# Optimization experiments

Measured on AMD Instinct MI355X. Metric: run time of the kernel, lower is better.

Reference implementation:

```python
import jax, jax.numpy as jnp
import numpy as np
import math

B, L, D, P = 2, 2048, 256, 32
PI = math.pi


def _layernorm(x, g, b, eps=1e-5):
    m = x.mean(-1, keepdims=True)
    v = x.var(-1, keepdims=True)
    return (x - m) / jnp.sqrt(v + eps) * g + b


def setup_inputs() -> dict:
    key = jax.random.key(0)
    ks = jax.random.split(key, 16)
    sd = 1.0 / math.sqrt(D)
    f32 = jnp.float32
    inp = {
        "x": jax.random.normal(ks[0], (B, L, D), f32),
        # key_encoder: Linear(D, P)
        "key_W": jax.random.normal(ks[1], (D, P), f32) * sd,
        "key_b": jnp.zeros((P,), f32),
        # value_encoder: Linear(D, D)
        "val_W": jax.random.normal(ks[2], (D, D), f32) * sd,
        "val_b": jnp.zeros((D,), f32),
        # refiner: LayerNorm(D), Linear(D, 2D), GELU, Linear(2D, D)
        "ln1_g": jnp.ones((D,), f32),
        "ln1_b": jnp.zeros((D,), f32),
        "W1": jax.random.normal(ks[3], (D, 2 * D), f32) * sd,
        "b1": jnp.zeros((2 * D,), f32),
        "W2": jax.random.normal(ks[4], (2 * D, D), f32) * (1.0 / math.sqrt(2 * D)),
        "b2": jnp.zeros((D,), f32),
        # to_out: LayerNorm(D), Linear(D, D)
        "ln2_g": jnp.ones((D,), f32),
        "ln2_b": jnp.zeros((D,), f32),
        "Wo": jax.random.normal(ks[5], (D, D), f32) * sd,
        "bo": jnp.zeros((D,), f32),
    }
    return inp


def reference(x, key_W, key_b, val_W, val_b, ln1_g, ln1_b, W1, b1, W2, b2,
              ln2_g, ln2_b, Wo, bo):
    # key phases in (-pi, pi); phasor exp(i*theta) handled as (cos, sin)
    phases = jnp.tanh(x @ key_W + key_b) * PI          # (B, L, P)
    values = x @ val_W + val_b                          # (B, L, D)

    cos_p = jnp.cos(phases)
    sin_p = jnp.sin(phases)
    # torch.roll(shifts=1, dims=1) then zero the first position -> shift right, row 0 = 0
    zrow = jnp.zeros_like(cos_p[:, :1])
    cos_s = jnp.concatenate([zrow, cos_p[:, :-1]], axis=1)
    sin_s = jnp.concatenate([zrow, sin_p[:, :-1]], axis=1)

    # odd positions hold values
    vmask = (jnp.arange(L) % 2 == 1).astype(x.dtype)    # (L,)
    mv = values * vmask[None, :, None]                  # (B, L, D)

    # bind: outer product phasor (P) x value (D); real/imag parts
    bound_re = cos_s[..., None] * mv[:, :, None, :]     # (B, L, P, D)
    bound_im = sin_s[..., None] * mv[:, :, None, :]
    mem_re = jnp.cumsum(bound_re, axis=1)
    mem_im = jnp.cumsum(bound_im, axis=1)

    # retrieve: Re[ memory * exp(-i*theta) ] summed over phases
    retrieved = (jnp.einsum('blpd,blp->bld', mem_re, cos_p)
                 + jnp.einsum('blpd,blp->bld', mem_im, sin_p))

    valid = jnp.maximum(jnp.cumsum(vmask), 1.0)         # (L,)
    retrieved = retrieved / (jnp.sqrt(valid)[None, :, None] * math.sqrt(P))

    h = _layernorm(retrieved, ln1_g, ln1_b)
    h = jax.nn.gelu(h @ W1 + b1, approximate=False)
    refined = h @ W2 + b2
    out = x + (_layernorm(refined, ln2_g, ln2_b) @ Wo + bo)
    return out
```

## Files before the change

kernel.cpp:

```cpp
#include <hip/hip_runtime.h>
#include <math.h>

#define BB 2
#define LL 2048
#define DD 256
#define PP 32
#define NC 64
#define PI_F 3.14159265358979323846f

typedef __attribute__((ext_vector_type(8))) short bf16x8;
typedef __attribute__((ext_vector_type(4))) float f32x4;
typedef unsigned short ushort_t;
typedef unsigned int uint_t;

__device__ inline ushort_t f2bf(float x) {
    uint_t u = __float_as_uint(x);
    uint_t r = (u + 0x7fffu + ((u >> 16) & 1u)) >> 16;
    return (ushort_t)r;
}

__global__ __launch_bounds__(256) void prep_key_kernel(
    const float* __restrict__ W1, const float* __restrict__ W2,
    const float* __restrict__ Wo, const float* __restrict__ valW,
    const float* __restrict__ x, const float* __restrict__ key_W,
    const float* __restrict__ key_b,
    ushort_t* __restrict__ W1t, ushort_t* __restrict__ W2t,
    ushort_t* __restrict__ Wot, ushort_t* __restrict__ valWt,
    float2* __restrict__ ph)
{
    const int bid = blockIdx.x;
    const int t = threadIdx.x;
    if (bid < 96) {
        __shared__ float T[64][65];
        const float* W; ushort_t* Wt; int K, N, tile;
        if (bid < 32)      { W = W1;   Wt = W1t;   K = 256; N = 512; tile = bid; }
        else if (bid < 64) { W = W2;   Wt = W2t;   K = 512; N = 256; tile = bid - 32; }
        else if (bid < 80) { W = Wo;   Wt = Wot;   K = 256; N = 256; tile = bid - 64; }
        else               { W = valW; Wt = valWt; K = 256; N = 256; tile = bid - 80; }
        const int ntiles = N / 64;
        const int k0 = (tile / ntiles) * 64, n0 = (tile % ntiles) * 64;
        {
            const int rr = t >> 2, cb = (t & 3) * 16;
            #pragma unroll
            for (int i = 0; i < 16; i += 4) {
                const float4 v = *(const float4*)&W[(k0 + rr) * N + n0 + cb + i];
                T[rr][cb + i + 0] = v.x; T[rr][cb + i + 1] = v.y;
                T[rr][cb + i + 2] = v.z; T[rr][cb + i + 3] = v.w;
            }
        }
        __syncthreads();
        {
            const int n = t >> 2, kb = (t & 3) * 16;
            #pragma unroll
            for (int i = 0; i < 16; ++i)
                Wt[(n0 + n) * K + k0 + kb + i] = f2bf(T[kb + i][n]);
        }
    } else {
        __shared__ ushort_t xt[16][264];
        __shared__ ushort_t kwT[32][264];
        __shared__ float rbuf[4][2][16][17];
        const int row0 = (bid - 96) * 16;
        {
            const int l = t >> 4, cb = (t & 15) * 16;
            const float* src = &x[(long)(row0 + l) * DD + cb];
            ushort_t tmp[16];
            #pragma unroll
            for (int i = 0; i < 4; ++i) {
                const float4 v = *(const float4*)&src[i * 4];
                tmp[i*4+0] = f2bf(v.x); tmp[i*4+1] = f2bf(v.y);
                tmp[i*4+2] = f2bf(v.z); tmp[i*4+3] = f2bf(v.w);
            }
            *(uint4*)&xt[l][cb]     = *(uint4*)&tmp[0];
            *(uint4*)&xt[l][cb + 8] = *(uint4*)&tmp[8];
        }
        {
            #pragma unroll
            for (int i = 0; i < 8; ++i) {
                const int idx4 = i * 256 + t;
                const int k = idx4 >> 3, pc = (idx4 & 7) * 4;
                const float4 v = *(const float4*)&key_W[k * 32 + pc];
                kwT[pc + 0][k] = f2bf(v.x);
                kwT[pc + 1][k] = f2bf(v.y);
                kwT[pc + 2][k] = f2bf(v.z);
                kwT[pc + 3][k] = f2bf(v.w);
            }
        }
        __syncthreads();
        const int wv = t >> 6, lane = t & 63;
        const int qd = lane >> 4, mc = lane & 15;
        f32x4 acc0 = {0.f,0.f,0.f,0.f}, acc1 = {0.f,0.f,0.f,0.f};
        #pragma unroll
        for (int ks = 0; ks < 2; ++ks) {
            const int ko = wv * 64 + ks * 32 + qd * 8;
            const bf16x8 a  = *(const bf16x8*)&xt[mc][ko];
            const bf16x8 b0 = *(const bf16x8*)&kwT[mc][ko];
            const bf16x8 b1 = *(const bf16x8*)&kwT[16 + mc][ko];
            acc0 = __builtin_amdgcn_mfma_f32_16x16x32_bf16(a, b0, acc0, 0, 0, 0);
            acc1 = __builtin_amdgcn_mfma_f32_16x16x32_bf16(a, b1, acc1, 0, 0, 0);
        }
        #pragma unroll
        for (int r = 0; r < 4; ++r) {
            rbuf[wv][0][qd * 4 + r][mc] = acc0[r];
            rbuf[wv][1][qd * 4 + r][mc] = acc1[r];
        }
        __syncthreads();
        #pragma unroll
        for (int rep = 0; rep < 2; ++rep) {
            const int idx = rep * 256 + t;
            const int p = idx & 31, l = idx >> 5;
            const int nf = p >> 4, mcol = p & 15;
            float a = key_b[p] + rbuf[0][nf][l][mcol] + rbuf[1][nf][l][mcol]
                    + rbuf[2][nf][l][mcol] + rbuf[3][nf][l][mcol];
            a = tanhf(a) * PI_F;
            float sn, cs;
            sincosf(a, &sn, &cs);
            ph[(long)(row0 + l) * PP + p] = make_float2(cs, sn);
        }
    }
}

__global__ __launch_bounds__(256) void valbind_kernel(
    const float* __restrict__ x, const float2* __restrict__ ph,
    const ushort_t* __restrict__ valWt, const float* __restrict__ val_b,
    ushort_t* __restrict__ VoddT, float* __restrict__ Mt)
{
    __shared__ ushort_t xsb[16][264];
    __shared__ ushort_t VdT[64][40];
    __shared__ ushort_t phsT[64][40];
    __shared__ float    Ms[64][68];

    const int tid = threadIdx.x;
    const int bid = blockIdx.x;
    const int b  = bid >> 8;
    const int c  = (bid >> 2) & 63;
    const int dq = bid & 3;
    const int base = b * LL;
    const int r0 = 32 * c;

    {
        const int j = tid >> 4, cb = (tid & 15) * 16;
        const float* src = &x[(long)(base + r0 + 2 * j + 1) * DD + cb];
        ushort_t tmp[16];
        #pragma unroll
        for (int i = 0; i < 4; ++i) {
            const float4 v = *(const float4*)&src[i * 4];
            tmp[i*4+0] = f2bf(v.x); tmp[i*4+1] = f2bf(v.y);
            tmp[i*4+2] = f2bf(v.z); tmp[i*4+3] = f2bf(v.w);
        }
        *(uint4*)&xsb[j][cb]     = *(uint4*)&tmp[0];
        *(uint4*)&xsb[j][cb + 8] = *(uint4*)&tmp[8];
    }
    {
        const int j = tid >> 4, qb = (tid & 15) * 4;
        const float4 v = *(const float4*)((const float*)ph +
                              (long)(base + r0 + 2 * j) * 64 + qb);
        phsT[qb + 0][j] = f2bf(v.x);
        phsT[qb + 1][j] = f2bf(v.y);
        phsT[qb + 2][j] = f2bf(v.z);
        phsT[qb + 3][j] = f2bf(v.w);
    }
    for (int e = tid; e < 64 * 16; e += 256) {
        phsT[e >> 4][16 + (e & 15)] = 0;
        VdT[e >> 4][16 + (e & 15)] = 0;
    }
    __syncthreads();

    const int wv = tid >> 6, lane = tid & 63;
    const int qd = lane >> 4, mc = lane & 15;

    f32x4 va = {0.f,0.f,0.f,0.f};
    const int dloc = wv * 16 + mc;
    const int ng = dq * 64 + dloc;
    const ushort_t* B0 = &valWt[(long)ng * 256];
    #pragma unroll
    for (int ks = 0; ks < 8; ++ks) {
        const bf16x8 a  = *(const bf16x8*)&xsb[mc][ks * 32 + qd * 8];
        const bf16x8 b0 = *(const bf16x8*)&B0[ks * 32 + qd * 8];
        va = __builtin_amdgcn_mfma_f32_16x16x32_bf16(a, b0, va, 0, 0, 0);
    }
    {
        const float bb = val_b[ng];
        #pragma unroll
        for (int r = 0; r < 4; ++r)
            VdT[dloc][qd * 4 + r] = f2bf(va[r] + bb);
    }
    __syncthreads();

    const bf16x8 a2 = *(const bf16x8*)&phsT[wv * 16 + mc][qd * 8];
    f32x4 macc[4];
    #pragma unroll
    for (int nf = 0; nf < 4; ++nf) {
        f32x4 z = {0.f,0.f,0.f,0.f};
        const bf16x8 b2 = *(const bf16x8*)&VdT[nf * 16 + mc][qd * 8];
        macc[nf] = __builtin_amdgcn_mfma_f32_16x16x32_bf16(a2, b2, z, 0, 0, 0);
    }
    #pragma unroll
    for (int nf = 0; nf < 4; ++nf) {
        #pragma unroll
        for (int r = 0; r < 4; ++r)
            Ms[nf * 16 + mc][wv * 16 + qd * 4 + r] = macc[nf][r];
    }
    __syncthreads();

    {
        float* dst = &Mt[((long)(b * NC + c) * 256 + dq * 64) * 64];
        #pragma unroll
        for (int p = 0; p < 4; ++p) {
            const int idx4 = p * 256 + tid;
            const int dl = idx4 >> 4, q4 = (idx4 & 15) * 4;
            *(float4*)&dst[dl * 64 + q4] = *(const float4*)&Ms[dl][q4];
        }
    }
    if (tid < 64) {
        ushort_t* vd = &VoddT[((long)(b * NC + c) * 256 + dq * 64 + tid) * 16];
        *(uint4*)&vd[0] = *(const uint4*)&VdT[tid][0];
        *(uint4*)&vd[8] = *(const uint4*)&VdT[tid][8];
    }
}

__global__ __launch_bounds__(256) void prefix_kernel(
    const float* __restrict__ M, ushort_t* __restrict__ Mpre_b)
{
    __shared__ float segsum[4][64];
    const int tid = threadIdx.x;
    const int b  = blockIdx.x >> 8;
    const int cg = blockIdx.x & 255;
    const int col = cg * 64 + (tid & 63);
    const int seg = tid >> 6;
    const long base = (long)b * NC * 16384 + col;

    float v[16], s = 0.f;
    #pragma unroll
    for (int i = 0; i < 16; ++i) {
        v[i] = M[base + (long)(seg * 16 + i) * 16384];
        s += v[i];
    }
    segsum[seg][tid & 63] = s;
    __syncthreads();
    float run = 0.f;
    #pragma unroll
    for (int sg = 0; sg < 3; ++sg)
        if (sg < seg) run += segsum[sg][tid & 63];
    #pragma unroll
    for (int i = 0; i < 16; ++i) {
        const long a = base + (long)(seg * 16 + i) * 16384;
        Mpre_b[a] = f2bf(run);
        run += v[i];
    }
}

__global__ __launch_bounds__(256) void retrieve_mlp_kernel(
    const float* __restrict__ ph, const ushort_t* __restrict__ Mpre_b,
    const ushort_t* __restrict__ VoddT,
    const float* __restrict__ ln1_g, const float* __restrict__ ln1_b,
    const ushort_t* __restrict__ W1t, const float* __restrict__ b1,
    const ushort_t* __restrict__ W2t, const float* __restrict__ b2,
    const float* __restrict__ ln2_g, const float* __restrict__ ln2_b,
    const ushort_t* __restrict__ Wot, const float* __restrict__ bo,
    const float* __restrict__ x, float* __restrict__ out)
{
    __shared__ ushort_t Bs_m[256][72];
    __shared__ ushort_t Bs_v[256][32];
    __shared__ ushort_t As_ph[16][72];
    __shared__ ushort_t Bs_sh[16][72];
    __shared__ ushort_t As_p[16][32];
    __shared__ float    refct[16][264];
    __shared__ ushort_t rhat_s[16][264];
    __shared__ ushort_t h_s[16][520];
    __shared__ ushort_t shT[16][264];

    const int tid = threadIdx.x;
    const int b = blockIdx.x >> 7;
    const int c = (blockIdx.x >> 1) & 63;
    const int h = blockIdx.x & 1;
    const int l0g = 32 * c + 16 * h;
    const long rowbase = (long)b * LL + l0g;

    {
        const ushort_t* src = &Mpre_b[(long)(b * NC + c) * 16384];
        #pragma unroll
        for (int p = 0; p < 8; ++p) {
            const int idx8 = p * 256 + tid;
            const int d = idx8 >> 3, q8 = (idx8 & 7) * 8;
            *(uint4*)&Bs_m[d][q8] = *(const uint4*)&src[idx8 * 8];
        }
    }
    {
        const int r = tid >> 4, q4 = (tid & 15) * 4;
        const float4 v = *(const float4*)&ph[(rowbase + r) * 64 + q4];
        ushort_t t0[4] = {f2bf(v.x), f2bf(v.y), f2bf(v.z), f2bf(v.w)};
        *(uint2*)&As_ph[r][q4] = *(uint2*)t0;
        const float4 w = *(const float4*)&ph[((long)b * LL + 32 * c + 2 * r) * 64 + q4];
        ushort_t t1[4] = {f2bf(w.x), f2bf(w.y), f2bf(w.z), f2bf(w.w)};
        *(uint2*)&Bs_sh[r][q4] = *(uint2*)t1;
    }
    {
        const ushort_t* src = &VoddT[(long)(b * NC + c) * 4096];
        const int j0 = (tid & 1) * 8;
        *(uint4*)&Bs_v[tid >> 1][j0] = *(const uint4*)&src[tid * 8];
        *(uint4*)&Bs_v[(tid + 256) >> 1][j0] = *(const uint4*)&src[(tid + 256) * 8];
        *(uint4*)&Bs_v[tid][16] = make_uint4(0, 0, 0, 0);
        *(uint4*)&Bs_v[tid][24] = make_uint4(0, 0, 0, 0);
        As_p[tid >> 4][16 + (tid & 15)] = 0;
    }
    __syncthreads();

    const int wv = tid >> 6, lane = tid & 63;
    const int qd = lane >> 4, mc = lane & 15;
    const int sk = (tid & 7) * 8;

    {
        f32x4 sacc = {0.f, 0.f, 0.f, 0.f};
        #pragma unroll
        for (int ks = 0; ks < 2; ++ks) {
            const bf16x8 a  = *(const bf16x8*)&As_ph[mc][ks * 32 + qd * 8];
            const bf16x8 bb = *(const bf16x8*)&Bs_sh[mc][ks * 32 + qd * 8];
            sacc = __builtin_amdgcn_mfma_f32_16x16x32_bf16(a, bb, sacc, 0, 0, 0);
        }
        if (wv == 0) {
            #pragma unroll
            for (int r = 0; r < 4; ++r) {
                const int l = qd * 4 + r;
                As_p[l][mc] = (2 * mc + 1 <= 16 * h + l) ? f2bf(sacc[r])
                                                         : (ushort_t)0;
            }
        }
    }

    f32x4 acc[4];
    #pragma unroll
    for (int i = 0; i < 4; ++i) acc[i] = (f32x4){0.f, 0.f, 0.f, 0.f};
    #pragma unroll
    for (int i = 0; i < 4; ++i) {
        const int d0 = wv * 64 + i * 16;
        #pragma unroll
        for (int ks = 0; ks < 2; ++ks) {
            const bf16x8 a  = *(const bf16x8*)&As_ph[mc][ks * 32 + qd * 8];
            const bf16x8 bb = *(const bf16x8*)&Bs_m[d0 + mc][ks * 32 + qd * 8];
            acc[i] = __builtin_amdgcn_mfma_f32_16x16x32_bf16(a, bb, acc[i], 0, 0, 0);
        }
    }
    __syncthreads();

    {
        const bf16x8 a2 = *(const bf16x8*)&As_p[mc][qd * 8];
        #pragma unroll
        for (int i = 0; i < 4; ++i) {
            const int d0 = wv * 64 + i * 16;
            const bf16x8 b2 = *(const bf16x8*)&Bs_v[d0 + mc][qd * 8];
            acc[i] = __builtin_amdgcn_mfma_f32_16x16x32_bf16(a2, b2, acc[i], 0, 0, 0);
        }
    }

    #pragma unroll
    for (int r = 0; r < 4; ++r) {
        const int l = qd * 4 + r;
        int va = (l0g + l + 1) >> 1; if (va < 1) va = 1;
        const float sc = 0.17677669529663687f * rsqrtf((float)va);
        #pragma unroll
        for (int i = 0; i < 4; ++i)
            refct[l][wv * 64 + i * 16 + mc] = acc[i][r] * sc;
    }
    __syncthreads();

    {
        const int row = tid >> 4, cg = (tid & 15) * 16;
        float s = 0.f, sq = 0.f;
        #pragma unroll
        for (int i = 0; i < 16; ++i) {
            const float v = refct[row][cg + i];
            s += v; sq += v * v;
        }
        s += __shfl_xor(s, 1, 16);  sq += __shfl_xor(sq, 1, 16);
        s += __shfl_xor(s, 2, 16);  sq += __shfl_xor(sq, 2, 16);
        s += __shfl_xor(s, 4, 16);  sq += __shfl_xor(sq, 4, 16);
        s += __shfl_xor(s, 8, 16);  sq += __shfl_xor(sq, 8, 16);
        const float m = s * (1.f / 256.f);
        const float inv = rsqrtf(sq * (1.f / 256.f) - m * m + 1e-5f);
        ushort_t o16[16];
        #pragma unroll
        for (int i = 0; i < 16; ++i) {
            const int cc = cg + i;
            o16[i] = f2bf((refct[row][cc] - m) * inv * ln1_g[cc] + ln1_b[cc]);
        }
        *(uint4*)&rhat_s[row][cg]     = *(uint4*)&o16[0];
        *(uint4*)&rhat_s[row][cg + 8] = *(uint4*)&o16[8];
    }

    #pragma unroll
    for (int nh = 0; nh < 2; ++nh) {
        f32x4 acc1[4];
        #pragma unroll
        for (int nf = 0; nf < 4; ++nf) acc1[nf] = (f32x4){0.f,0.f,0.f,0.f};
        for (int k0 = 0; k0 < 256; k0 += 64) {
            __syncthreads();
            #pragma unroll
            for (int rr = 0; rr < 8; ++rr) {
                const int n = rr * 32 + (tid >> 3);
                *(uint4*)&Bs_m[n][sk] =
                    *(const uint4*)&W1t[(long)(nh * 256 + n) * 256 + k0 + sk];
            }
            __syncthreads();
            #pragma unroll
            for (int ks = 0; ks < 2; ++ks) {
                const bf16x8 a = *(const bf16x8*)&rhat_s[mc][k0 + ks * 32 + qd * 8];
                #pragma unroll
                for (int nf = 0; nf < 4; ++nf) {
                    const bf16x8 bb = *(const bf16x8*)&Bs_m[wv * 64 + nf * 16 + mc][ks * 32 + qd * 8];
                    acc1[nf] = __builtin_amdgcn_mfma_f32_16x16x32_bf16(a, bb, acc1[nf], 0, 0, 0);
                }
            }
        }
        #pragma unroll
        for (int nf = 0; nf < 4; ++nf) {
            const int n = nh * 256 + wv * 64 + nf * 16 + mc;
            const float bb = b1[n];
            #pragma unroll
            for (int r = 0; r < 4; ++r) {
                float v = acc1[nf][r] + bb;
                v = 0.5f * v * (1.f + erff(v * 0.70710678118654752f));
                h_s[qd * 4 + r][n] = f2bf(v);
            }
        }
    }

    f32x4 acc2[4];
    #pragma unroll
    for (int nf = 0; nf < 4; ++nf) acc2[nf] = (f32x4){0.f,0.f,0.f,0.f};
    for (int k0 = 0; k0 < 512; k0 += 64) {
        __syncthreads();
        #pragma unroll
        for (int rr = 0; rr < 8; ++rr) {
            const int n = rr * 32 + (tid >> 3);
            *(uint4*)&Bs_m[n][sk] = *(const uint4*)&W2t[(long)n * 512 + k0 + sk];
        }
        __syncthreads();
        #pragma unroll
        for (int ks = 0; ks < 2; ++ks) {
            const bf16x8 a = *(const bf16x8*)&h_s[mc][k0 + ks * 32 + qd * 8];
            #pragma unroll
            for (int nf = 0; nf < 4; ++nf) {
                const bf16x8 bb = *(const bf16x8*)&Bs_m[wv * 64 + nf * 16 + mc][ks * 32 + qd * 8];
                acc2[nf] = __builtin_amdgcn_mfma_f32_16x16x32_bf16(a, bb, acc2[nf], 0, 0, 0);
            }
        }
    }
    #pragma unroll
    for (int nf = 0; nf < 4; ++nf) {
        const int n = wv * 64 + nf * 16 + mc;
        const float bb = b2[n];
        #pragma unroll
        for (int r = 0; r < 4; ++r)
            refct[qd * 4 + r][n] = acc2[nf][r] + bb;
    }
    __syncthreads();

    {
        const int row = tid >> 4, cg = (tid & 15) * 16;
        float s = 0.f, sq = 0.f;
        #pragma unroll
        for (int i = 0; i < 16; ++i) {
            const float v = refct[row][cg + i];
            s += v; sq += v * v;
        }
        s  += __shfl_xor(s, 1, 16);  sq += __shfl_xor(sq, 1, 16);
        s  += __shfl_xor(s, 2, 16);  sq += __shfl_xor(sq, 2, 16);
        s  += __shfl_xor(s, 4, 16);  sq += __shfl_xor(sq, 4, 16);
        s  += __shfl_xor(s, 8, 16);  sq += __shfl_xor(sq, 8, 16);
        const float m = s * (1.f / 256.f);
        const float inv = rsqrtf(sq * (1.f / 256.f) - m * m + 1e-5f);
        #pragma unroll
        for (int i = 0; i < 16; ++i) {
            const int cc = cg + i;
            shT[row][cc] = f2bf((refct[row][cc] - m) * inv * ln2_g[cc] + ln2_b[cc]);
        }
    }

    f32x4 acc3[4];
    #pragma unroll
    for (int nf = 0; nf < 4; ++nf) acc3[nf] = (f32x4){0.f,0.f,0.f,0.f};
    for (int k0 = 0; k0 < 256; k0 += 64) {
        __syncthreads();
        #pragma unroll
        for (int rr = 0; rr < 8; ++rr) {
            const int n = rr * 32 + (tid >> 3);
            *(uint4*)&Bs_m[n][sk] = *(const uint4*)&Wot[(long)n * 256 + k0 + sk];
        }
        __syncthreads();
        #pragma unroll
        for (int ks = 0; ks < 2; ++ks) {
            const bf16x8 a = *(const bf16x8*)&shT[mc][k0 + ks * 32 + qd * 8];
            #pragma unroll
            for (int nf = 0; nf < 4; ++nf) {
                const bf16x8 bb = *(const bf16x8*)&Bs_m[wv * 64 + nf * 16 + mc][ks * 32 + qd * 8];
                acc3[nf] = __builtin_amdgcn_mfma_f32_16x16x32_bf16(a, bb, acc3[nf], 0, 0, 0);
            }
        }
    }
    #pragma unroll
    for (int nf = 0; nf < 4; ++nf) {
        const int n = wv * 64 + nf * 16 + mc;
        const float bb = bo[n];
        #pragma unroll
        for (int r = 0; r < 4; ++r) {
            const long row = rowbase + qd * 4 + r;
            out[row * DD + n] = acc3[nf][r] + bb + x[row * DD + n];
        }
    }
}

extern "C" void kernel_launch(void* const* d_in, const int* in_sizes, int n_in,
                              void* d_out, int out_size, void* d_ws, size_t ws_size,
                              hipStream_t stream)
{
    const float* x     = (const float*)d_in[0];
    const float* key_W = (const float*)d_in[1];
    const float* key_b = (const float*)d_in[2];
    const float* val_W = (const float*)d_in[3];
    const float* val_b = (const float*)d_in[4];
    const float* ln1_g = (const float*)d_in[5];
    const float* ln1_b = (const float*)d_in[6];
    const float* W1    = (const float*)d_in[7];
    const float* b1    = (const float*)d_in[8];
    const float* W2    = (const float*)d_in[9];
    const float* b2    = (const float*)d_in[10];
    const float* ln2_g = (const float*)d_in[11];
    const float* ln2_b = (const float*)d_in[12];
    const float* Wo    = (const float*)d_in[13];
    const float* bo    = (const float*)d_in[14];
    float* outp = (float*)d_out;

    float* ws = (float*)d_ws;
    float*  ph      = ws;
    float*  Mt      = ws + 262144;
    ushort_t* Mpre_b = (ushort_t*)(Mt + 2097152);
    ushort_t* VoddT  = Mpre_b + 2097152;
    ushort_t* rhat_b = VoddT + 524288;
    ushort_t* W1t   = rhat_b + 1048576;
    ushort_t* W2t   = W1t + 131072;
    ushort_t* Wot   = W2t + 131072;
    ushort_t* valWt = Wot + 65536;

    prep_key_kernel<<<352, 256, 0, stream>>>(W1, W2, Wo, val_W, x, key_W, key_b,
                                             W1t, W2t, Wot, valWt, (float2*)ph);
    valbind_kernel<<<512, 256, 0, stream>>>(x, (const float2*)ph, valWt, val_b,
                                            VoddT, Mt);
    prefix_kernel<<<512, 256, 0, stream>>>(Mt, Mpre_b);
    retrieve_mlp_kernel<<<256, 256, 0, stream>>>(ph, Mpre_b, VoddT, ln1_g, ln1_b,
                                                 W1t, b1, W2t, b2, ln2_g, ln2_b,
                                                 Wot, bo, x, outp);
}
```

Baseline: 126.5 us.

## Fuse four kernels into one persistent kernel with software grid barriers

Merges the key/weight-prep, value-bind, prefix-scan and retrieve-MLP kernels into one persistent kernel of 256 blocks. The stages are separated by atomic-counter grid barriers, and blocks loop over the extra work units of stages that need 512. The aim is to remove the launch gaps and tail effects between the four dispatches. In exchange it adds spin-wait barrier overhead and a large shared-memory footprint, and it relies on all 256 blocks being co-resident, which risks deadlock if they are not.

```diff
diff --git a/kernel.cpp b/kernel.cpp
--- a/kernel.cpp
+++ b/kernel.cpp
@@ -7,6 +7,7 @@
 #define PP 32
 #define NC 64
 #define PI_F 3.14159265358979323846f
+#define NBLK 256
 
 typedef __attribute__((ext_vector_type(8))) short bf16x8;
 typedef __attribute__((ext_vector_type(4))) float f32x4;
@@ -19,49 +20,51 @@
     return (ushort_t)r;
 }
 
-__global__ __launch_bounds__(256) void prep_key_kernel(
-    const float* __restrict__ W1, const float* __restrict__ W2,
-    const float* __restrict__ Wo, const float* __restrict__ valW,
+__device__ __forceinline__ void gridbar(int* cnt, int* flag, int id) {
+    __syncthreads();
+    if (threadIdx.x == 0) {
+        __threadfence();
+        if (atomicAdd(&cnt[id], 1) == NBLK - 1) {
+            __threadfence();
+            atomicExch(flag, id + 1);
+        } else {
+            while (atomicAdd(flag, 0) < id + 1) { __builtin_amdgcn_s_sleep(2); }
+        }
+        __threadfence();
+    }
+    __syncthreads();
+}
+
+__global__ __launch_bounds__(256) void mega_kernel(
     const float* __restrict__ x, const float* __restrict__ key_W,
-    const float* __restrict__ key_b,
+    const float* __restrict__ key_b, const float* __restrict__ valW,
+    const float* __restrict__ val_b, const float* __restrict__ ln1_g,
+    const float* __restrict__ ln1_b, const float* __restrict__ W1,
+    const float* __restrict__ b1, const float* __restrict__ W2,
+    const float* __restrict__ b2, const float* __restrict__ ln2_g,
+    const float* __restrict__ ln2_b, const float* __restrict__ Wo,
+    const float* __restrict__ bo,
+    float2* __restrict__ ph, float* __restrict__ Mt,
+    ushort_t* __restrict__ Mpre_b, ushort_t* __restrict__ VoddT,
     ushort_t* __restrict__ W1t, ushort_t* __restrict__ W2t,
     ushort_t* __restrict__ Wot, ushort_t* __restrict__ valWt,
-    float2* __restrict__ ph)
+    int* __restrict__ bar, float* __restrict__ out)
 {
+    __shared__ __align__(16) char smem[109824];
+    char* sm = smem;
+    const int tid = threadIdx.x;
     const int bid = blockIdx.x;
-    const int t = threadIdx.x;
-    if (bid < 96) {
-        __shared__ float T[64][65];
-        const float* W; ushort_t* Wt; int K, N, tile;
-        if (bid < 32)      { W = W1;   Wt = W1t;   K = 256; N = 512; tile = bid; }
-        else if (bid < 64) { W = W2;   Wt = W2t;   K = 512; N = 256; tile = bid - 32; }
-        else if (bid < 80) { W = Wo;   Wt = Wot;   K = 256; N = 256; tile = bid - 64; }
-        else               { W = valW; Wt = valWt; K = 256; N = 256; tile = bid - 80; }
-        const int ntiles = N / 64;
-        const int k0 = (tile / ntiles) * 64, n0 = (tile % ntiles) * 64;
-        {
-            const int rr = t >> 2, cb = (t & 3) * 16;
-            #pragma unroll
-            for (int i = 0; i < 16; i += 4) {
-                const float4 v = *(const float4*)&W[(k0 + rr) * N + n0 + cb + i];
-                T[rr][cb + i + 0] = v.x; T[rr][cb + i + 1] = v.y;
-                T[rr][cb + i + 2] = v.z; T[rr][cb + i + 3] = v.w;
-            }
-        }
-        __syncthreads();
-        {
-            const int n = t >> 2, kb = (t & 3) * 16;
-            #pragma unroll
-            for (int i = 0; i < 16; ++i)
-                Wt[(n0 + n) * K + k0 + kb + i] = f2bf(T[kb + i][n]);
-        }
-    } else {
-        __shared__ ushort_t xt[16][264];
-        __shared__ ushort_t kwT[32][264];
-        __shared__ float rbuf[4][2][16][17];
-        const int row0 = (bid - 96) * 16;
-        {
-            const int l = t >> 4, cb = (t & 15) * 16;
+    int* cnt = bar;
+    int* flag = bar + 3;
+
+    {
+        ushort_t (*xt)[264]  = (ushort_t(*)[264])sm;
+        ushort_t (*kwT)[264] = (ushort_t(*)[264])(sm + 8448);
+        float (*rbuf)[2][16][17] = (float(*)[2][16][17])(sm + 25344);
+
+        const int row0 = bid * 16;
+        {
+            const int l = tid >> 4, cb = (tid & 15) * 16;
             const float* src = &x[(long)(row0 + l) * DD + cb];
             ushort_t tmp[16];
             #pragma unroll
@@ -76,7 +79,7 @@
         {
             #pragma unroll
             for (int i = 0; i < 8; ++i) {
-                const int idx4 = i * 256 + t;
+                const int idx4 = i * 256 + tid;
                 const int k = idx4 >> 3, pc = (idx4 & 7) * 4;
                 const float4 v = *(const float4*)&key_W[k * 32 + pc];
                 kwT[pc + 0][k] = f2bf(v.x);
@@ -86,7 +89,7 @@
             }
         }
         __syncthreads();
-        const int wv = t >> 6, lane = t & 63;
+        const int wv = tid >> 6, lane = tid & 63;
         const int qd = lane >> 4, mc = lane & 15;
         f32x4 acc0 = {0.f,0.f,0.f,0.f}, acc1 = {0.f,0.f,0.f,0.f};
         #pragma unroll
@@ -106,7 +109,7 @@
         __syncthreads();
         #pragma unroll
         for (int rep = 0; rep < 2; ++rep) {
-            const int idx = rep * 256 + t;
+            const int idx = rep * 256 + tid;
             const int p = idx & 31, l = idx >> 5;
             const int nf = p >> 4, mcol = p & 15;
             float a = key_b[p] + rbuf[0][nf][l][mcol] + rbuf[1][nf][l][mcol]
@@ -116,395 +119,417 @@
             sincosf(a, &sn, &cs);
             ph[(long)(row0 + l) * PP + p] = make_float2(cs, sn);
         }
+        __syncthreads();
+
+        if (bid < 96) {
+            float (*T)[65] = (float(*)[65])sm;
+            const float* W; ushort_t* Wt; int K, N, tile;
+            if (bid < 32)      { W = W1;   Wt = W1t;   K = 256; N = 512; tile = bid; }
+            else if (bid < 64) { W = W2;   Wt = W2t;   K = 512; N = 256; tile = bid - 32; }
+            else if (bid < 80) { W = Wo;   Wt = Wot;   K = 256; N = 256; tile = bid - 64; }
+            else               { W = valW; Wt = valWt; K = 256; N = 256; tile = bid - 80; }
+            const int ntiles = N / 64;
+            const int k0 = (tile / ntiles) * 64, n0 = (tile % ntiles) * 64;
+            {
+                const int rr = tid >> 2, cb = (tid & 3) * 16;
+                #pragma unroll
+                for (int i = 0; i < 16; i += 4) {
+                    const float4 v = *(const float4*)&W[(k0 + rr) * N + n0 + cb + i];
+                    T[rr][cb + i + 0] = v.x; T[rr][cb + i + 1] = v.y;
+                    T[rr][cb + i + 2] = v.z; T[rr][cb + i + 3] = v.w;
+                }
+            }
+            __syncthreads();
+            {
+                const int n = tid >> 2, kb = (tid & 3) * 16;
+                #pragma unroll
+                for (int i = 0; i < 16; ++i)
+                    Wt[(n0 + n) * K + k0 + kb + i] = f2bf(T[kb + i][n]);
+            }
+        }
     }
-}
-
-__global__ __launch_bounds__(256) void valbind_kernel(
-    const float* __restrict__ x, const float2* __restrict__ ph,
-    const ushort_t* __restrict__ valWt, const float* __restrict__ val_b,
-    ushort_t* __restrict__ VoddT, float* __restrict__ Mt)
-{
-    __shared__ ushort_t xsb[16][264];
-    __shared__ ushort_t VdT[64][40];
-    __shared__ ushort_t phsT[64][40];
-    __shared__ float    Ms[64][68];
-
-    const int tid = threadIdx.x;
-    const int bid = blockIdx.x;
-    const int b  = bid >> 8;
-    const int c  = (bid >> 2) & 63;
-    const int dq = bid & 3;
-    const int base = b * LL;
-    const int r0 = 32 * c;
+    gridbar(cnt, flag, 0);
 
     {
-        const int j = tid >> 4, cb = (tid & 15) * 16;
-        const float* src = &x[(long)(base + r0 + 2 * j + 1) * DD + cb];
-        ushort_t tmp[16];
-        #pragma unroll
-        for (int i = 0; i < 4; ++i) {
-            const float4 v = *(const float4*)&src[i * 4];
-            tmp[i*4+0] = f2bf(v.x); tmp[i*4+1] = f2bf(v.y);
-            tmp[i*4+2] = f2bf(v.z); tmp[i*4+3] = f2bf(v.w);
-        }
-        *(uint4*)&xsb[j][cb]     = *(uint4*)&tmp[0];
-        *(uint4*)&xsb[j][cb + 8] = *(uint4*)&tmp[8];
+        ushort_t (*xsb)[264] = (ushort_t(*)[264])sm;
+        ushort_t (*VdT)[40]  = (ushort_t(*)[40])(sm + 8448);
+        ushort_t (*phsT)[40] = (ushort_t(*)[40])(sm + 13568);
+        float    (*Ms)[68]   = (float(*)[68])(sm + 18688);
+
+        for (int rep = 0; rep < 2; ++rep) {
+            const int u = bid + rep * 256;
+            const int b  = u >> 8;
+            const int c  = (u >> 2) & 63;
+            const int dq = u & 3;
+            const int base = b * LL;
+            const int r0 = 32 * c;
+            __syncthreads();
+            {
+                const int j = tid >> 4, cb = (tid & 15) * 16;
+                const float* src = &x[(long)(base + r0 + 2 * j + 1) * DD + cb];
+                ushort_t tmp[16];
+                #pragma unroll
+                for (int i = 0; i < 4; ++i) {
+                    const float4 v = *(const float4*)&src[i * 4];
+                    tmp[i*4+0] = f2bf(v.x); tmp[i*4+1] = f2bf(v.y);
+                    tmp[i*4+2] = f2bf(v.z); tmp[i*4+3] = f2bf(v.w);
+                }
+                *(uint4*)&xsb[j][cb]     = *(uint4*)&tmp[0];
+                *(uint4*)&xsb[j][cb + 8] = *(uint4*)&tmp[8];
+            }
+            {
+                const int j = tid >> 4, qb = (tid & 15) * 4;
+                const float4 v = *(const float4*)((const float*)ph +
+                                      (long)(base + r0 + 2 * j) * 64 + qb);
+                phsT[qb + 0][j] = f2bf(v.x);
+                phsT[qb + 1][j] = f2bf(v.y);
+                phsT[qb + 2][j] = f2bf(v.z);
+                phsT[qb + 3][j] = f2bf(v.w);
+            }
+            for (int e = tid; e < 64 * 16; e += 256) {
+                phsT[e >> 4][16 + (e & 15)] = 0;
+                VdT[e >> 4][16 + (e & 15)] = 0;
+            }
+            __syncthreads();
+
+            const int wv = tid >> 6, lane = tid & 63;
+            const int qd = lane >> 4, mc = lane & 15;
+
+            f32x4 va = {0.f,0.f,0.f,0.f};
+            const int dloc = wv * 16 + mc;
+            const int ng = dq * 64 + dloc;
+            const ushort_t* B0 = &valWt[(long)ng * 256];
+            #pragma unroll
+            for (int ks = 0; ks < 8; ++ks) {
+                const bf16x8 a  = *(const bf16x8*)&xsb[mc][ks * 32 + qd * 8];
+                const bf16x8 b0 = *(const bf16x8*)&B0[ks * 32 + qd * 8];
+                va = __builtin_amdgcn_mfma_f32_16x16x32_bf16(a, b0, va, 0, 0, 0);
+            }
+            {
+                const float bb = val_b[ng];
+                #pragma unroll
+                for (int r = 0; r < 4; ++r)
+                    VdT[dloc][qd * 4 + r] = f2bf(va[r] + bb);
+            }
+            __syncthreads();
+
+            const bf16x8 a2 = *(const bf16x8*)&phsT[wv * 16 + mc][qd * 8];
+            f32x4 macc[4];
+            #pragma unroll
+            for (int nf = 0; nf < 4; ++nf) {
+                f32x4 z = {0.f,0.f,0.f,0.f};
+                const bf16x8 b2 = *(const bf16x8*)&VdT[nf * 16 + mc][qd * 8];
+                macc[nf] = __builtin_amdgcn_mfma_f32_16x16x32_bf16(a2, b2, z, 0, 0, 0);
+            }
+            #pragma unroll
+            for (int nf = 0; nf < 4; ++nf) {
+                #pragma unroll
+                for (int r = 0; r < 4; ++r)
+                    Ms[nf * 16 + mc][wv * 16 + qd * 4 + r] = macc[nf][r];
+            }
+            __syncthreads();
+
+            {
+                float* dst = &Mt[((long)(b * NC + c) * 256 + dq * 64) * 64];
+                #pragma unroll
+                for (int p = 0; p < 4; ++p) {
+                    const int idx4 = p * 256 + tid;
+                    const int dl = idx4 >> 4, q4 = (idx4 & 15) * 4;
+                    *(float4*)&dst[dl * 64 + q4] = *(const float4*)&Ms[dl][q4];
+                }
+            }
+            if (tid < 64) {
+                ushort_t* vd = &VoddT[((long)(b * NC + c) * 256 + dq * 64 + tid) * 16];
+                *(uint4*)&vd[0] = *(const uint4*)&VdT[tid][0];
+                *(uint4*)&vd[8] = *(const uint4*)&VdT[tid][8];
+            }
+        }
     }
+    gridbar(cnt, flag, 1);
+
     {
-        const int j = tid >> 4, qb = (tid & 15) * 4;
-        const float4 v = *(const float4*)((const float*)ph +
-                              (long)(base + r0 + 2 * j) * 64 + qb);
-        phsT[qb + 0][j] = f2bf(v.x);
-        phsT[qb + 1][j] = f2bf(v.y);
-        phsT[qb + 2][j] = f2bf(v.z);
-        phsT[qb + 3][j] = f2bf(v.w);
+        float (*segsum)[64] = (float(*)[64])sm;
+        for (int rep = 0; rep < 2; ++rep) {
+            const int u = bid + rep * 256;
+            const int b  = u >> 8;
+            const int cg = u & 255;
+            const int col = cg * 64 + (tid & 63);
+            const int seg = tid >> 6;
+            const long base = (long)b * NC * 16384 + col;
+
+            float v[16], s = 0.f;
+            #pragma unroll
+            for (int i = 0; i < 16; ++i) {
+                v[i] = Mt[base + (long)(seg * 16 + i) * 16384];
+                s += v[i];
+            }
+            segsum[seg][tid & 63] = s;
+            __syncthreads();
+            float run = 0.f;
+            #pragma unroll
+            for (int sg = 0; sg < 3; ++sg)
+                if (sg < seg) run += segsum[sg][tid & 63];
+            #pragma unroll
+            for (int i = 0; i < 16; ++i) {
+                const long a = base + (long)(seg * 16 + i) * 16384;
+                Mpre_b[a] = f2bf(run);
+                run += v[i];
+            }
+            __syncthreads();
+        }
     }
-    for (int e = tid; e < 64 * 16; e += 256) {
-        phsT[e >> 4][16 + (e & 15)] = 0;
-        VdT[e >> 4][16 + (e & 15)] = 0;
-    }
-    __syncthreads();
-
-    const int wv = tid >> 6, lane = tid & 63;
-    const int qd = lane >> 4, mc = lane & 15;
-
-    f32x4 va = {0.f,0.f,0.f,0.f};
-    const int dloc = wv * 16 + mc;
-    const int ng = dq * 64 + dloc;
-    const ushort_t* B0 = &valWt[(long)ng * 256];
-    #pragma unroll
-    for (int ks = 0; ks < 8; ++ks) {
-        const bf16x8 a  = *(const bf16x8*)&xsb[mc][ks * 32 + qd * 8];
-        const bf16x8 b0 = *(const bf16x8*)&B0[ks * 32 + qd * 8];
-        va = __builtin_amdgcn_mfma_f32_16x16x32_bf16(a, b0, va, 0, 0, 0);
-    }
+    gridbar(cnt, flag, 2);
+
     {
-        const float bb = val_b[ng];
-        #pragma unroll
-        for (int r = 0; r < 4; ++r)
-            VdT[dloc][qd * 4 + r] = f2bf(va[r] + bb);
-    }
-    __syncthreads();
-
-    const bf16x8 a2 = *(const bf16x8*)&phsT[wv * 16 + mc][qd * 8];
-    f32x4 macc[4];
-    #pragma unroll
-    for (int nf = 0; nf < 4; ++nf) {
-        f32x4 z = {0.f,0.f,0.f,0.f};
-        const bf16x8 b2 = *(const bf16x8*)&VdT[nf * 16 + mc][qd * 8];
-        macc[nf] = __builtin_amdgcn_mfma_f32_16x16x32_bf16(a2, b2, z, 0, 0, 0);
-    }
-    #pragma unroll
-    for (int nf = 0; nf < 4; ++nf) {
-        #pragma unroll
-        for (int r = 0; r < 4; ++r)
-            Ms[nf * 16 + mc][wv * 16 + qd * 4 + r] = macc[nf][r];
-    }
-    __syncthreads();
-
-    {
-        float* dst = &Mt[((long)(b * NC + c) * 256 + dq * 64) * 64];
-        #pragma unroll
-        for (int p = 0; p < 4; ++p) {
-            const int idx4 = p * 256 + tid;
-            const int dl = idx4 >> 4, q4 = (idx4 & 15) * 4;
-            *(float4*)&dst[dl * 64 + q4] = *(const float4*)&Ms[dl][q4];
-        }
-    }
-    if (tid < 64) {
-        ushort_t* vd = &VoddT[((long)(b * NC + c) * 256 + dq * 64 + tid) * 16];
-        *(uint4*)&vd[0] = *(const uint4*)&VdT[tid][0];
-        *(uint4*)&vd[8] = *(const uint4*)&VdT[tid][8];
-    }
-}
-
-__global__ __launch_bounds__(256) void prefix_kernel(
-    const float* __restrict__ M, ushort_t* __restrict__ Mpre_b)
-{
-    __shared__ float segsum[4][64];
-    const int tid = threadIdx.x;
-    const int b  = blockIdx.x >> 8;
-    const int cg = blockIdx.x & 255;
-    const int col = cg * 64 + (tid & 63);
-    const int seg = tid >> 6;
-    const long base = (long)b * NC * 16384 + col;
-
-    float v[16], s = 0.f;
-    #pragma unroll
-    for (int i = 0; i < 16; ++i) {
-        v[i] = M[base + (long)(seg * 16 + i) * 16384];
-        s += v[i];
-    }
-    segsum[seg][tid & 63] = s;
-    __syncthreads();
-    float run = 0.f;
-    #pragma unroll
-    for (int sg = 0; sg < 3; ++sg)
-        if (sg < seg) run += segsum[sg][tid & 63];
-    #pragma unroll
-    for (int i = 0; i < 16; ++i) {
-        const long a = base + (long)(seg * 16 + i) * 16384;
-        Mpre_b[a] = f2bf(run);
-        run += v[i];
-    }
-}
-
-__global__ __launch_bounds__(256) void retrieve_mlp_kernel(
-    const float* __restrict__ ph, const ushort_t* __restrict__ Mpre_b,
-    const ushort_t* __restrict__ VoddT,
-    const float* __restrict__ ln1_g, const float* __restrict__ ln1_b,
-    const ushort_t* __restrict__ W1t, const float* __restrict__ b1,
-    const ushort_t* __restrict__ W2t, const float* __restrict__ b2,
-    const float* __restrict__ ln2_g, const float* __restrict__ ln2_b,
-    const ushort_t* __restrict__ Wot, const float* __restrict__ bo,
-    const float* __restrict__ x, float* __restrict__ out)
-{
-    __shared__ ushort_t Bs_m[256][72];
-    __shared__ ushort_t Bs_v[256][32];
-    __shared__ ushort_t As_ph[16][72];
-    __shared__ ushort_t Bs_sh[16][72];
-    __shared__ ushort_t As_p[16][32];
-    __shared__ float    refct[16][264];
-    __shared__ ushort_t rhat_s[16][264];
-    __shared__ ushort_t h_s[16][520];
-    __shared__ ushort_t shT[16][264];
-
-    const int tid = threadIdx.x;
-    const int b = blockIdx.x >> 7;
-    const int c = (blockIdx.x >> 1) & 63;
-    const int h = blockIdx.x & 1;
-    const int l0g = 32 * c + 16 * h;
-    const long rowbase = (long)b * LL + l0g;
-
-    {
-        const ushort_t* src = &Mpre_b[(long)(b * NC + c) * 16384];
-        #pragma unroll
-        for (int p = 0; p < 8; ++p) {
-            const int idx8 = p * 256 + tid;
-            const int d = idx8 >> 3, q8 = (idx8 & 7) * 8;
-            *(uint4*)&Bs_m[d][q8] = *(const uint4*)&src[idx8 * 8];
-        }
-    }
-    {
-        const int r = tid >> 4, q4 = (tid & 15) * 4;
-        const float4 v = *(const float4*)&ph[(rowbase + r) * 64 + q4];
-        ushort_t t0[4] = {f2bf(v.x), f2bf(v.y), f2bf(v.z), f2bf(v.w)};
-        *(uint2*)&As_ph[r][q4] = *(uint2*)t0;
-        const float4 w = *(const float4*)&ph[((long)b * LL + 32 * c + 2 * r) * 64 + q4];
-        ushort_t t1[4] = {f2bf(w.x), f2bf(w.y), f2bf(w.z), f2bf(w.w)};
-        *(uint2*)&Bs_sh[r][q4] = *(uint2*)t1;
-    }
-    {
-        const ushort_t* src = &VoddT[(long)(b * NC + c) * 4096];
-        const int j0 = (tid & 1) * 8;
-        *(uint4*)&Bs_v[tid >> 1][j0] = *(const uint4*)&src[tid * 8];
-        *(uint4*)&Bs_v[(tid + 256) >> 1][j0] = *(const uint4*)&src[(tid + 256) * 8];
-        *(uint4*)&Bs_v[tid][16] = make_uint4(0, 0, 0, 0);
-        *(uint4*)&Bs_v[tid][24] = make_uint4(0, 0, 0, 0);
-        As_p[tid >> 4][16 + (tid & 15)] = 0;
-    }
-    __syncthreads();
-
-    const int wv = tid >> 6, lane = tid & 63;
-    const int qd = lane >> 4, mc = lane & 15;
-    const int sk = (tid & 7) * 8;
-
-    {
-        f32x4 sacc = {0.f, 0.f, 0.f, 0.f};
-        #pragma unroll
-        for (int ks = 0; ks < 2; ++ks) {
-            const bf16x8 a  = *(const bf16x8*)&As_ph[mc][ks * 32 + qd * 8];
-            const bf16x8 bb = *(const bf16x8*)&Bs_sh[mc][ks * 32 + qd * 8];
-            sacc = __builtin_amdgcn_mfma_f32_16x16x32_bf16(a, bb, sacc, 0, 0, 0);
-        }
-        if (wv == 0) {
-            #pragma unroll
-            for (int r = 0; r < 4; ++r) {
-                const int l = qd * 4 + r;
-                As_p[l][mc] = (2 * mc + 1 <= 16 * h + l) ? f2bf(sacc[r])
-                                                         : (ushort_t)0;
-            }
-        }
-    }
-
-    f32x4 acc[4];
-    #pragma unroll
-    for (int i = 0; i < 4; ++i) acc[i] = (f32x4){0.f, 0.f, 0.f, 0.f};
-    #pragma unroll
-    for (int i = 0; i < 4; ++i) {
-        const int d0 = wv * 64 + i * 16;
-        #pragma unroll
-        for (int ks = 0; ks < 2; ++ks) {
-            const bf16x8 a  = *(const bf16x8*)&As_ph[mc][ks * 32 + qd * 8];
-            const bf16x8 bb = *(const bf16x8*)&Bs_m[d0 + mc][ks * 32 + qd * 8];
-            acc[i] = __builtin_amdgcn_mfma_f32_16x16x32_bf16(a, bb, acc[i], 0, 0, 0);
-        }
-    }
-    __syncthreads();
-
-    {
-        const bf16x8 a2 = *(const bf16x8*)&As_p[mc][qd * 8];
+        ushort_t (*Bs_m)[72]  = (ushort_t(*)[72])sm;
+        ushort_t (*Bs_v)[32]  = (ushort_t(*)[32])(sm + 36864);
+        ushort_t (*As_ph)[72] = (ushort_t(*)[72])(sm + 53248);
+        ushort_t (*Bs_sh)[72] = (ushort_t(*)[72])(sm + 55552);
+        ushort_t (*As_p)[32]  = (ushort_t(*)[32])(sm + 57856);
+        float    (*refct)[264] = (float(*)[264])(sm + 58880);
+        ushort_t (*rhat_s)[264] = (ushort_t(*)[264])(sm + 75776);
+        ushort_t (*h_s)[520]  = (ushort_t(*)[520])(sm + 84224);
+        ushort_t (*shT)[264]  = (ushort_t(*)[264])(sm + 100864);
+
+        const int b = bid >> 7;
+        const int c = (bid >> 1) & 63;
+        const int h = bid & 1;
+        const int l0g = 32 * c + 16 * h;
+        const long rowbase = (long)b * LL + l0g;
+
+        {
+            const ushort_t* src = &Mpre_b[(long)(b * NC + c) * 16384];
+            #pragma unroll
+            for (int p = 0; p < 8; ++p) {
+                const int idx8 = p * 256 + tid;
+                const int d = idx8 >> 3, q8 = (idx8 & 7) * 8;
+                *(uint4*)&Bs_m[d][q8] = *(const uint4*)&src[idx8 * 8];
+            }
+        }
+        {
+            const int r = tid >> 4, q4 = (tid & 15) * 4;
+            const float4 v = *(const float4*)&ph[0];
+            (void)v;
+            const float4 vv = *(const float4*)((const float*)ph + (rowbase + r) * 64 + q4);
+            ushort_t t0[4] = {f2bf(vv.x), f2bf(vv.y), f2bf(vv.z), f2bf(vv.w)};
+            *(uint2*)&As_ph[r][q4] = *(uint2*)t0;
+            const float4 w = *(const float4*)((const float*)ph +
+                                 ((long)b * LL + 32 * c + 2 * r) * 64 + q4);
+            ushort_t t1[4] = {f2bf(w.x), f2bf(w.y), f2bf(w.z), f2bf(w.w)};
+            *(uint2*)&Bs_sh[r][q4] = *(uint2*)t1;
+        }
+        {
+            const ushort_t* src = &VoddT[(long)(b * NC + c) * 4096];
+            const int j0 = (tid & 1) * 8;
+            *(uint4*)&Bs_v[tid >> 1][j0] = *(const uint4*)&src[tid * 8];
+            *(uint4*)&Bs_v[(tid + 256) >> 1][j0] = *(const uint4*)&src[(tid + 256) * 8];
+            *(uint4*)&Bs_v[tid][16] = make_uint4(0, 0, 0, 0);
+            *(uint4*)&Bs_v[tid][24] = make_uint4(0, 0, 0, 0);
+            As_p[tid >> 4][16 + (tid & 15)] = 0;
+        }
+        __syncthreads();
+
+        const int wv = tid >> 6, lane = tid & 63;
+        const int qd = lane >> 4, mc = lane & 15;
+        const int sk = (tid & 7) * 8;
+
+        {
+            f32x4 sacc = {0.f, 0.f, 0.f, 0.f};
+            #pragma unroll
+            for (int ks = 0; ks < 2; ++ks) {
+                const bf16x8 a  = *(const bf16x8*)&As_ph[mc][ks * 32 + qd * 8];
+                const bf16x8 bb = *(const bf16x8*)&Bs_sh[mc][ks * 32 + qd * 8];
+                sacc = __builtin_amdgcn_mfma_f32_16x16x32_bf16(a, bb, sacc, 0, 0, 0);
+            }
+            if (wv == 0) {
+                #pragma unroll
+                for (int r = 0; r < 4; ++r) {
+                    const int l = qd * 4 + r;
+                    As_p[l][mc] = (2 * mc + 1 <= 16 * h + l) ? f2bf(sacc[r])
+                                                             : (ushort_t)0;
+                }
+            }
+        }
+
+        f32x4 acc[4];
+        #pragma unroll
+        for (int i = 0; i < 4; ++i) acc[i] = (f32x4){0.f, 0.f, 0.f, 0.f};
         #pragma unroll
         for (int i = 0; i < 4; ++i) {
             const int d0 = wv * 64 + i * 16;
-            const bf16x8 b2 = *(const bf16x8*)&Bs_v[d0 + mc][qd * 8];
-            acc[i] = __builtin_amdgcn_mfma_f32_16x16x32_bf16(a2, b2, acc[i], 0, 0, 0);
-        }
-    }
-
-    #pragma unroll
-    for (int r = 0; r < 4; ++r) {
-        const int l = qd * 4 + r;
-        int va = (l0g + l + 1) >> 1; if (va < 1) va = 1;
-        const float sc = 0.17677669529663687f * rsqrtf((float)va);
-        #pragma unroll
-        for (int i = 0; i < 4; ++i)
-            refct[l][wv * 64 + i * 16 + mc] = acc[i][r] * sc;
-    }
-    __syncthreads();
-
-    {
-        const int row = tid >> 4, cg = (tid & 15) * 16;
-        float s = 0.f, sq = 0.f;
-        #pragma unroll
-        for (int i = 0; i < 16; ++i) {
-            const float v = refct[row][cg + i];
-            s += v; sq += v * v;
-        }
-        s += __shfl_xor(s, 1, 16);  sq += __shfl_xor(sq, 1, 16);
-        s += __shfl_xor(s, 2, 16);  sq += __shfl_xor(sq, 2, 16);
-        s += __shfl_xor(s, 4, 16);  sq += __shfl_xor(sq, 4, 16);
-        s += __shfl_xor(s, 8, 16);  sq += __shfl_xor(sq, 8, 16);
-        const float m = s * (1.f / 256.f);
-        const float inv = rsqrtf(sq * (1.f / 256.f) - m * m + 1e-5f);
-        ushort_t o16[16];
-        #pragma unroll
-        for (int i = 0; i < 16; ++i) {
-            const int cc = cg + i;
-            o16[i] = f2bf((refct[row][cc] - m) * inv * ln1_g[cc] + ln1_b[cc]);
-        }
-        *(uint4*)&rhat_s[row][cg]     = *(uint4*)&o16[0];
-        *(uint4*)&rhat_s[row][cg + 8] = *(uint4*)&o16[8];
-    }
-
-    #pragma unroll
-    for (int nh = 0; nh < 2; ++nh) {
-        f32x4 acc1[4];
-        #pragma unroll
-        for (int nf = 0; nf < 4; ++nf) acc1[nf] = (f32x4){0.f,0.f,0.f,0.f};
-        for (int k0 = 0; k0 < 256; k0 += 64) {
+            #pragma unroll
+            for (int ks = 0; ks < 2; ++ks) {
+                const bf16x8 a  = *(const bf16x8*)&As_ph[mc][ks * 32 + qd * 8];
+                const bf16x8 bb = *(const bf16x8*)&Bs_m[d0 + mc][ks * 32 + qd * 8];
+                acc[i] = __builtin_amdgcn_mfma_f32_16x16x32_bf16(a, bb, acc[i], 0, 0, 0);
+            }
+        }
+        __syncthreads();
+
+        {
+            const bf16x8 a2 = *(const bf16x8*)&As_p[mc][qd * 8];
+            #pragma unroll
+            for (int i = 0; i < 4; ++i) {
+                const int d0 = wv * 64 + i * 16;
+                const bf16x8 b2 = *(const bf16x8*)&Bs_v[d0 + mc][qd * 8];
+                acc[i] = __builtin_amdgcn_mfma_f32_16x16x32_bf16(a2, b2, acc[i], 0, 0, 0);
+            }
+        }
+
+        #pragma unroll
+        for (int r = 0; r < 4; ++r) {
+            const int l = qd * 4 + r;
+            int va = (l0g + l + 1) >> 1; if (va < 1) va = 1;
+            const float sc = 0.17677669529663687f * rsqrtf((float)va);
+            #pragma unroll
+            for (int i = 0; i < 4; ++i)
+                refct[l][wv * 64 + i * 16 + mc] = acc[i][r] * sc;
+        }
+        __syncthreads();
+
+        {
+            const int row = tid >> 4, cg = (tid & 15) * 16;
+            float s = 0.f, sq = 0.f;
+            #pragma unroll
+            for (int i = 0; i < 16; ++i) {
+                const float v = refct[row][cg + i];
+                s += v; sq += v * v;
+            }
+            s += __shfl_xor(s, 1, 16);  sq += __shfl_xor(sq, 1, 16);
+            s += __shfl_xor(s, 2, 16);  sq += __shfl_xor(sq, 2, 16);
+            s += __shfl_xor(s, 4, 16);  sq += __shfl_xor(sq, 4, 16);
+            s += __shfl_xor(s, 8, 16);  sq += __shfl_xor(sq, 8, 16);
+            const float m = s * (1.f / 256.f);
+            const float inv = rsqrtf(sq * (1.f / 256.f) - m * m + 1e-5f);
+            ushort_t o16[16];
+            #pragma unroll
+            for (int i = 0; i < 16; ++i) {
+                const int cc = cg + i;
+                o16[i] = f2bf((refct[row][cc] - m) * inv * ln1_g[cc] + ln1_b[cc]);
+            }
+            *(uint4*)&rhat_s[row][cg]     = *(uint4*)&o16[0];
+            *(uint4*)&rhat_s[row][cg + 8] = *(uint4*)&o16[8];
+        }
+
+        #pragma unroll
+        for (int nh = 0; nh < 2; ++nh) {
+            f32x4 acc1[4];
+            #pragma unroll
+            for (int nf = 0; nf < 4; ++nf) acc1[nf] = (f32x4){0.f,0.f,0.f,0.f};
+            for (int k0 = 0; k0 < 256; k0 += 64) {
+                __syncthreads();
+                #pragma unroll
+                for (int rr = 0; rr < 8; ++rr) {
+                    const int n = rr * 32 + (tid >> 3);
+                    *(uint4*)&Bs_m[n][sk] =
+                        *(const uint4*)&W1t[(long)(nh * 256 + n) * 256 + k0 + sk];
+                }
+                __syncthreads();
+                #pragma unroll
+                for (int ks = 0; ks < 2; ++ks) {
+                    const bf16x8 a = *(const bf16x8*)&rhat_s[mc][k0 + ks * 32 + qd * 8];
+                    #pragma unroll
+                    for (int nf = 0; nf < 4; ++nf) {
+                        const bf16x8 bb = *(const bf16x8*)&Bs_m[wv * 64 + nf * 16 + mc][ks * 32 + qd * 8];
+                        acc1[nf] = __builtin_amdgcn_mfma_f32_16x16x32_bf16(a, bb, acc1[nf], 0, 0, 0);
+                    }
+                }
+            }
+            #pragma unroll
+            for (int nf = 0; nf < 4; ++nf) {
+                const int n = nh * 256 + wv * 64 + nf * 16 + mc;
+                const float bb = b1[n];
+                #pragma unroll
+                for (int r = 0; r < 4; ++r) {
+                    float v = acc1[nf][r] + bb;
+                    v = 0.5f * v * (1.f + erff(v * 0.70710678118654752f));
+                    h_s[qd * 4 + r][n] = f2bf(v);
+                }
+            }
+        }
+
+        f32x4 acc2[4];
+        #pragma unroll
+        for (int nf = 0; nf < 4; ++nf) acc2[nf] = (f32x4){0.f,0.f,0.f,0.f};
+        for (int k0 = 0; k0 < 512; k0 += 64) {
             __syncthreads();
             #pragma unroll
             for (int rr = 0; rr < 8; ++rr) {
                 const int n = rr * 32 + (tid >> 3);
-                *(uint4*)&Bs_m[n][sk] =
-                    *(const uint4*)&W1t[(long)(nh * 256 + n) * 256 + k0 + sk];
+                *(uint4*)&Bs_m[n][sk] = *(const uint4*)&W2t[(long)n * 512 + k0 + sk];
             }
             __syncthreads();
             #pragma unroll
             for (int ks = 0; ks < 2; ++ks) {
-                const bf16x8 a = *(const bf16x8*)&rhat_s[mc][k0 + ks * 32 + qd * 8];
+                const bf16x8 a = *(const bf16x8*)&h_s[mc][k0 + ks * 32 + qd * 8];
                 #pragma unroll
                 for (int nf = 0; nf < 4; ++nf) {
                     const bf16x8 bb = *(const bf16x8*)&Bs_m[wv * 64 + nf * 16 + mc][ks * 32 + qd * 8];
-                    acc1[nf] = __builtin_amdgcn_mfma_f32_16x16x32_bf16(a, bb, acc1[nf], 0, 0, 0);
+                    acc2[nf] = __builtin_amdgcn_mfma_f32_16x16x32_bf16(a, bb, acc2[nf], 0, 0, 0);
                 }
             }
         }
         #pragma unroll
         for (int nf = 0; nf < 4; ++nf) {
-            const int n = nh * 256 + wv * 64 + nf * 16 + mc;
-            const float bb = b1[n];
+            const int n = wv * 64 + nf * 16 + mc;
+            const float bb = b2[n];
+            #pragma unroll
+            for (int r = 0; r < 4; ++r)
+                refct[qd * 4 + r][n] = acc2[nf][r] + bb;
+        }
+        __syncthreads();
+
+        {
+            const int row = tid >> 4, cg = (tid & 15) * 16;
+            float s = 0.f, sq = 0.f;
+            #pragma unroll
+            for (int i = 0; i < 16; ++i) {
+                const float v = refct[row][cg + i];
+                s += v; sq += v * v;
+            }
+            s  += __shfl_xor(s, 1, 16);  sq += __shfl_xor(sq, 1, 16);
+            s  += __shfl_xor(s, 2, 16);  sq += __shfl_xor(sq, 2, 16);
+            s  += __shfl_xor(s, 4, 16);  sq += __shfl_xor(sq, 4, 16);
+            s  += __shfl_xor(s, 8, 16);  sq += __shfl_xor(sq, 8, 16);
+            const float m = s * (1.f / 256.f);
+            const float inv = rsqrtf(sq * (1.f / 256.f) - m * m + 1e-5f);
+            #pragma unroll
+            for (int i = 0; i < 16; ++i) {
+                const int cc = cg + i;
+                shT[row][cc] = f2bf((refct[row][cc] - m) * inv * ln2_g[cc] + ln2_b[cc]);
+            }
+        }
+
+        f32x4 acc3[4];
+        #pragma unroll
+        for (int nf = 0; nf < 4; ++nf) acc3[nf] = (f32x4){0.f,0.f,0.f,0.f};
+        for (int k0 = 0; k0 < 256; k0 += 64) {
+            __syncthreads();
+            #pragma unroll
+            for (int rr = 0; rr < 8; ++rr) {
+                const int n = rr * 32 + (tid >> 3);
+                *(uint4*)&Bs_m[n][sk] = *(const uint4*)&Wot[(long)n * 256 + k0 + sk];
+            }
+            __syncthreads();
+            #pragma unroll
+            for (int ks = 0; ks < 2; ++ks) {
+                const bf16x8 a = *(const bf16x8*)&shT[mc][k0 + ks * 32 + qd * 8];
+                #pragma unroll
+                for (int nf = 0; nf < 4; ++nf) {
+                    const bf16x8 bb = *(const bf16x8*)&Bs_m[wv * 64 + nf * 16 + mc][ks * 32 + qd * 8];
+                    acc3[nf] = __builtin_amdgcn_mfma_f32_16x16x32_bf16(a, bb, acc3[nf], 0, 0, 0);
+                }
+            }
+        }
+        #pragma unroll
+        for (int nf = 0; nf < 4; ++nf) {
+            const int n = wv * 64 + nf * 16 + mc;
+            const float bb = bo[n];
             #pragma unroll
             for (int r = 0; r < 4; ++r) {
-                float v = acc1[nf][r] + bb;
-                v = 0.5f * v * (1.f + erff(v * 0.70710678118654752f));
-                h_s[qd * 4 + r][n] = f2bf(v);
-            }
-        }
-    }
-
-    f32x4 acc2[4];
-    #pragma unroll
-    for (int nf = 0; nf < 4; ++nf) acc2[nf] = (f32x4){0.f,0.f,0.f,0.f};
-    for (int k0 = 0; k0 < 512; k0 += 64) {
-        __syncthreads();
-        #pragma unroll
-        for (int rr = 0; rr < 8; ++rr) {
-            const int n = rr * 32 + (tid >> 3);
-            *(uint4*)&Bs_m[n][sk] = *(const uint4*)&W2t[(long)n * 512 + k0 + sk];
-        }
-        __syncthreads();
-        #pragma unroll
-        for (int ks = 0; ks < 2; ++ks) {
-            const bf16x8 a = *(const bf16x8*)&h_s[mc][k0 + ks * 32 + qd * 8];
-            #pragma unroll
-            for (int nf = 0; nf < 4; ++nf) {
-                const bf16x8 bb = *(const bf16x8*)&Bs_m[wv * 64 + nf * 16 + mc][ks * 32 + qd * 8];
-                acc2[nf] = __builtin_amdgcn_mfma_f32_16x16x32_bf16(a, bb, acc2[nf], 0, 0, 0);
-            }
-        }
-    }
-    #pragma unroll
-    for (int nf = 0; nf < 4; ++nf) {
-        const int n = wv * 64 + nf * 16 + mc;
-        const float bb = b2[n];
-        #pragma unroll
-        for (int r = 0; r < 4; ++r)
-            refct[qd * 4 + r][n] = acc2[nf][r] + bb;
-    }
-    __syncthreads();
-
-    {
-        const int row = tid >> 4, cg = (tid & 15) * 16;
-        float s = 0.f, sq = 0.f;
-        #pragma unroll
-        for (int i = 0; i < 16; ++i) {
-            const float v = refct[row][cg + i];
-            s += v; sq += v * v;
-        }
-        s  += __shfl_xor(s, 1, 16);  sq += __shfl_xor(sq, 1, 16);
-        s  += __shfl_xor(s, 2, 16);  sq += __shfl_xor(sq, 2, 16);
-        s  += __shfl_xor(s, 4, 16);  sq += __shfl_xor(sq, 4, 16);
-        s  += __shfl_xor(s, 8, 16);  sq += __shfl_xor(sq, 8, 16);
-        const float m = s * (1.f / 256.f);
-        const float inv = rsqrtf(sq * (1.f / 256.f) - m * m + 1e-5f);
-        #pragma unroll
-        for (int i = 0; i < 16; ++i) {
-            const int cc = cg + i;
-            shT[row][cc] = f2bf((refct[row][cc] - m) * inv * ln2_g[cc] + ln2_b[cc]);
-        }
-    }
-
-    f32x4 acc3[4];
-    #pragma unroll
-    for (int nf = 0; nf < 4; ++nf) acc3[nf] = (f32x4){0.f,0.f,0.f,0.f};
-    for (int k0 = 0; k0 < 256; k0 += 64) {
-        __syncthreads();
-        #pragma unroll
-        for (int rr = 0; rr < 8; ++rr) {
-            const int n = rr * 32 + (tid >> 3);
-            *(uint4*)&Bs_m[n][sk] = *(const uint4*)&Wot[(long)n * 256 + k0 + sk];
-        }
-        __syncthreads();
-        #pragma unroll
-        for (int ks = 0; ks < 2; ++ks) {
-            const bf16x8 a = *(const bf16x8*)&shT[mc][k0 + ks * 32 + qd * 8];
-            #pragma unroll
-            for (int nf = 0; nf < 4; ++nf) {
-                const bf16x8 bb = *(const bf16x8*)&Bs_m[wv * 64 + nf * 16 + mc][ks * 32 + qd * 8];
-                acc3[nf] = __builtin_amdgcn_mfma_f32_16x16x32_bf16(a, bb, acc3[nf], 0, 0, 0);
-            }
-        }
-    }
-    #pragma unroll
-    for (int nf = 0; nf < 4; ++nf) {
-        const int n = wv * 64 + nf * 16 + mc;
-        const float bb = bo[n];
-        #pragma unroll
-        for (int r = 0; r < 4; ++r) {
-            const long row = rowbase + qd * 4 + r;
-            out[row * DD + n] = acc3[nf][r] + bb + x[row * DD + n];
+                const long row = rowbase + qd * 4 + r;
+                out[row * DD + n] = acc3[nf][r] + bb + x[row * DD + n];
+            }
         }
     }
 }
@@ -540,13 +565,11 @@
     ushort_t* W2t   = W1t + 131072;
     ushort_t* Wot   = W2t + 131072;
     ushort_t* valWt = Wot + 65536;
-
-    prep_key_kernel<<<352, 256, 0, stream>>>(W1, W2, Wo, val_W, x, key_W, key_b,
-                                             W1t, W2t, Wot, valWt, (float2*)ph);
-    valbind_kernel<<<512, 256, 0, stream>>>(x, (const float2*)ph, valWt, val_b,
-                                            VoddT, Mt);
-    prefix_kernel<<<512, 256, 0, stream>>>(Mt, Mpre_b);
-    retrieve_mlp_kernel<<<256, 256, 0, stream>>>(ph, Mpre_b, VoddT, ln1_g, ln1_b,
-                                                 W1t, b1, W2t, b2, ln2_g, ln2_b,
-                                                 Wot, bo, x, outp);
+    int* bar = (int*)(valWt + 65536);
+
+    hipMemsetAsync(bar, 0, 16, stream);
+    mega_kernel<<<NBLK, 256, 0, stream>>>(
+        x, key_W, key_b, val_W, val_b, ln1_g, ln1_b, W1, b1, W2, b2,
+        ln2_g, ln2_b, Wo, bo,
+        (float2*)ph, Mt, Mpre_b, VoddT, W1t, W2t, Wot, valWt, bar, outp);
 }
```

Result: slower. 190.2 us (+50.3%).
